# Optimization experiments

Measured on AMD Instinct MI355X. Metric: run time of the kernel, lower is better.

The kernel has to match this reference:

```python
import jax, jax.numpy as jnp
import numpy as np

N_NODES = 50000
N_EDGES = 800000
NUM_FEATURES = 256
HIDDEN = 256
HEADS = 8
OUT_DIM = 2


def setup_inputs() -> dict:
    key = jax.random.key(0)
    ks = jax.random.split(key, 16)
    C1 = HIDDEN // HEADS  # 32 per-head channels
    inp = {
        'x': jax.random.normal(ks[0], (N_NODES, NUM_FEATURES), dtype=jnp.float32),
        'edge_index': jax.random.randint(ks[1], (2, N_EDGES), 0, N_NODES, dtype=jnp.int64),
        # layer 1: num_features -> heads * (hidden//heads)
        'W1': jax.random.normal(ks[2], (NUM_FEATURES, HEADS * C1), dtype=jnp.float32) * 0.05,
        'att_src1': jax.random.normal(ks[3], (HEADS, C1), dtype=jnp.float32) * 0.1,
        'att_dst1': jax.random.normal(ks[4], (HEADS, C1), dtype=jnp.float32) * 0.1,
        'b1': jnp.zeros((HEADS * C1,), dtype=jnp.float32),
        # layer 2: hidden -> heads * (hidden//heads)
        'W2': jax.random.normal(ks[5], (HIDDEN, HEADS * C1), dtype=jnp.float32) * 0.05,
        'att_src2': jax.random.normal(ks[6], (HEADS, C1), dtype=jnp.float32) * 0.1,
        'att_dst2': jax.random.normal(ks[7], (HEADS, C1), dtype=jnp.float32) * 0.1,
        'b2': jnp.zeros((HEADS * C1,), dtype=jnp.float32),
        # layer 3: hidden -> output_dim, heads=1, concat=False
        'W3': jax.random.normal(ks[8], (HIDDEN, OUT_DIM), dtype=jnp.float32) * 0.05,
        'att_src3': jax.random.normal(ks[9], (1, OUT_DIM), dtype=jnp.float32) * 0.1,
        'att_dst3': jax.random.normal(ks[10], (1, OUT_DIM), dtype=jnp.float32) * 0.1,
        'b3': jnp.zeros((OUT_DIM,), dtype=jnp.float32),
    }
    return inp


def _gat_layer(x, src, dst, W, a_src, a_dst, b, concat):
    # PyG GATConv: h = x W -> [N, H, C]; e_ij = leaky_relu(a_src.h_j + a_dst.h_i)
    # softmax over edges grouped by destination, then scatter-add h_j * alpha.
    N = x.shape[0]
    H, C = a_src.shape
    h = (x @ W).reshape(N, H, C)
    alpha_s = jnp.einsum('nhc,hc->nh', h, a_src)  # [N, H]
    alpha_d = jnp.einsum('nhc,hc->nh', h, a_dst)
    e = jax.nn.leaky_relu(alpha_s[src] + alpha_d[dst], negative_slope=0.2)  # [E, H]
    m = jax.ops.segment_max(e, dst, num_segments=N)  # per-dst max for stable softmax
    ee = jnp.exp(e - m[dst])
    denom = jax.ops.segment_sum(ee, dst, num_segments=N)
    alpha = ee / (denom[dst] + 1e-16)  # [E, H]
    msg = h[src] * alpha[:, :, None]  # [E, H, C]
    out = jax.ops.segment_sum(msg, dst, num_segments=N)  # [N, H, C]
    out = out.reshape(N, H * C) if concat else out.mean(axis=1)
    return out + b


def reference(x, edge_index, W1, att_src1, att_dst1, b1, W2, att_src2, att_dst2, b2, W3, att_src3, att_dst3, b3):
    N = x.shape[0]
    loops = jnp.arange(N, dtype=edge_index.dtype)
    src = jnp.concatenate([edge_index[0], loops])  # PyG add_self_loops=True
    dst = jnp.concatenate([edge_index[1], loops])
    h = _gat_layer(x, src, dst, W1, att_src1, att_dst1, b1, concat=True)
    h = jax.nn.elu(h)  # dropout is identity in eval mode
    h = _gat_layer(h, src, dst, W2, att_src2, att_dst2, b2, concat=True)
    h = jax.nn.elu(h)
    out = _gat_layer(h, src, dst, W3, att_src3, att_dst3, b3, concat=False)
    return out  # [N, output_dim]; batch=None so pooling/MLP head is skipped
```

## Files before the change

### kernel.cpp

```cpp
#include <hip/hip_runtime.h>
#include <math.h>

#define NF 256
#define NHEADS 8
#define MNEG -1e30f

typedef _Float16 half8 __attribute__((ext_vector_type(8)));
typedef float f32x4 __attribute__((ext_vector_type(4)));


__global__ __launch_bounds__(256) void deg_count_k(const int* __restrict__ dst, int* __restrict__ deg, int E) {
    int i = (blockIdx.x * 256 + threadIdx.x) * 4;
    if (i + 4 <= E) {
        int4 d = *(const int4*)&dst[i];
        atomicAdd(&deg[d.x], 1);
        atomicAdd(&deg[d.y], 1);
        atomicAdd(&deg[d.z], 1);
        atomicAdd(&deg[d.w], 1);
    } else {
        for (int e = i; e < E; ++e) atomicAdd(&deg[dst[e]], 1);
    }
}

__global__ __launch_bounds__(256) void scan1_k(const int* __restrict__ deg, int* __restrict__ indptr,
                                               int* __restrict__ bsum, int n) {
    __shared__ int sh[256];
    int tid = threadIdx.x;
    int i = blockIdx.x * 256 + tid;
    int d = (i < n) ? deg[i] : 0;
    sh[tid] = d;
    __syncthreads();
#pragma unroll
    for (int off = 1; off < 256; off <<= 1) {
        int t = (tid >= off) ? sh[tid - off] : 0;
        __syncthreads();
        sh[tid] += t;
        __syncthreads();
    }
    if (i < n) indptr[i] = sh[tid] - d;
    if (tid == 255) bsum[blockIdx.x] = sh[255];
}

__global__ __launch_bounds__(256) void scan3_k(const int* __restrict__ deg, int* __restrict__ indptr,
                                               const int* __restrict__ bsum, int* __restrict__ cursor,
                                               int* __restrict__ srcs, int n, int nb) {
    __shared__ int sh[256];
    int tid = threadIdx.x;
    int d = (tid < nb) ? bsum[tid] : 0;
    sh[tid] = d;
    __syncthreads();
#pragma unroll
    for (int off = 1; off < 256; off <<= 1) {
        int t = (tid >= off) ? sh[tid - off] : 0;
        __syncthreads();
        sh[tid] += t;
        __syncthreads();
    }
    int bid = blockIdx.x;
    int boff = sh[bid] - ((bid < nb) ? bsum[bid] : 0);
    int i = bid * 256 + tid;
    if (i < n) {
        int v = indptr[i] + boff + i;
        indptr[i] = v;
        srcs[v] = i;
        cursor[i] = v + 1;
        if (i == n - 1) indptr[n] = v + deg[i] + 1;
    }
}

__global__ __launch_bounds__(256) void fill_edge_k(const int* __restrict__ esrc, const int* __restrict__ edst,
                                                   int* __restrict__ cursor, int* __restrict__ srcs, int E) {
    int i = (blockIdx.x * 256 + threadIdx.x) * 4;
    if (i + 4 <= E) {
        int4 s = *(const int4*)&esrc[i];
        int4 d = *(const int4*)&edst[i];
        srcs[atomicAdd(&cursor[d.x], 1)] = s.x;
        srcs[atomicAdd(&cursor[d.y], 1)] = s.y;
        srcs[atomicAdd(&cursor[d.z], 1)] = s.z;
        srcs[atomicAdd(&cursor[d.w], 1)] = s.w;
    } else {
        for (int e = i; e < E; ++e) srcs[atomicAdd(&cursor[edst[e]], 1)] = esrc[e];
    }
}


__global__ __launch_bounds__(256) void prep_w_k(const float* __restrict__ W1, const float* __restrict__ W2,
                                                _Float16* __restrict__ O1, _Float16* __restrict__ O2) {
    int tid = blockIdx.x * 256 + threadIdx.x;
    const float* W = (tid < 65536) ? W1 : W2;
    _Float16* O = (tid < 65536) ? O1 : O2;
    int t = tid & 65535;
    int k = t >> 8, c = t & 255;
    O[(size_t)c * 256 + k] = (_Float16)W[t];
}


template <int AF32>
__global__ __launch_bounds__(512, 4) void gemm_mfma_k(const void* __restrict__ Av, const _Float16* __restrict__ WTh,
                                                      const float* __restrict__ att_s, const float* __restrict__ att_d,
                                                      _Float16* __restrict__ C, float* __restrict__ aS,
                                                      float* __restrict__ aD, int M) {
    __shared__ __align__(16) _Float16 Asub[2][128][40];
    __shared__ __align__(16) _Float16 Wsub[2][256][40];
    int t = threadIdx.x;
    int wave = t >> 6, lane = t & 63;
    int wm = wave >> 2, wn = wave & 3;
    int lr = lane & 15, lg = lane >> 4;
    int r0 = blockIdx.x * 128;
    const float* Af = (const float*)Av;
    const _Float16* Ah = (const _Float16*)Av;

    int arow = t >> 2, aoff = (t & 3) * 8;
    int wcol = t >> 1, woff = (t & 1) * 16;
    int ga_row = r0 + arow; ga_row = ga_row < M ? ga_row : M - 1;

    half8 aR, wR0, wR1;
    {
        if (AF32) {
            const float* p = Af + (size_t)ga_row * 256 + aoff;
            float4 x0 = *(const float4*)p;
            float4 x1 = *(const float4*)(p + 4);
            aR[0] = (_Float16)x0.x; aR[1] = (_Float16)x0.y; aR[2] = (_Float16)x0.z; aR[3] = (_Float16)x0.w;
            aR[4] = (_Float16)x1.x; aR[5] = (_Float16)x1.y; aR[6] = (_Float16)x1.z; aR[7] = (_Float16)x1.w;
        } else {
            aR = *(const half8*)(Ah + (size_t)ga_row * 256 + aoff);
        }
        const _Float16* p = WTh + (size_t)wcol * 256 + woff;
        wR0 = *(const half8*)p;
        wR1 = *(const half8*)(p + 8);
    }
    *(half8*)&Asub[0][arow][aoff] = aR;
    *(half8*)&Wsub[0][wcol][woff] = wR0;
    *(half8*)&Wsub[0][wcol][woff + 8] = wR1;
    __syncthreads();

    f32x4 acc[4][4];
#pragma unroll
    for (int mr = 0; mr < 4; ++mr)
#pragma unroll
        for (int nr = 0; nr < 4; ++nr) acc[mr][nr] = (f32x4){0.f, 0.f, 0.f, 0.f};

#pragma unroll
    for (int ks = 0; ks < 8; ++ks) {
        int cur = ks & 1;
        if (ks < 7) {
            int k0 = (ks + 1) * 32;
            if (AF32) {
                const float* p = Af + (size_t)ga_row * 256 + k0 + aoff;
                float4 x0 = *(const float4*)p;
                float4 x1 = *(const float4*)(p + 4);
                aR[0] = (_Float16)x0.x; aR[1] = (_Float16)x0.y; aR[2] = (_Float16)x0.z; aR[3] = (_Float16)x0.w;
                aR[4] = (_Float16)x1.x; aR[5] = (_Float16)x1.y; aR[6] = (_Float16)x1.z; aR[7] = (_Float16)x1.w;
            } else {
                aR = *(const half8*)(Ah + (size_t)ga_row * 256 + k0 + aoff);
            }
            const _Float16* p = WTh + (size_t)wcol * 256 + k0 + woff;
            wR0 = *(const half8*)p;
            wR1 = *(const half8*)(p + 8);
        }
        {
            half8 a[4], b[4];
#pragma unroll
            for (int mr = 0; mr < 4; ++mr)
                a[mr] = *(const half8*)&Asub[cur][wm * 64 + mr * 16 + lr][lg * 8];
#pragma unroll
            for (int nr = 0; nr < 4; ++nr)
                b[nr] = *(const half8*)&Wsub[cur][wn * 64 + nr * 16 + lr][lg * 8];
#pragma unroll
            for (int mr = 0; mr < 4; ++mr)
#pragma unroll
                for (int nr = 0; nr < 4; ++nr)
                    acc[mr][nr] = __builtin_amdgcn_mfma_f32_16x16x32_f16(a[mr], b[nr], acc[mr][nr], 0, 0, 0);
        }
        if (ks < 7) {
            __syncthreads();
            *(half8*)&Asub[cur ^ 1][arow][aoff] = aR;
            *(half8*)&Wsub[cur ^ 1][wcol][woff] = wR0;
            *(half8*)&Wsub[cur ^ 1][wcol][woff + 8] = wR1;
            __syncthreads();
        }
    }

    int c0 = wn * 64;
    int h0 = wn * 2, h1 = wn * 2 + 1;
    float as_c0 = att_s[h0 * 32 + lr],      as_c1 = att_s[h0 * 32 + 16 + lr];
    float as_c2 = att_s[h1 * 32 + lr],      as_c3 = att_s[h1 * 32 + 16 + lr];
    float ad_c0 = att_d[h0 * 32 + lr],      ad_c1 = att_d[h0 * 32 + 16 + lr];
    float ad_c2 = att_d[h1 * 32 + lr],      ad_c3 = att_d[h1 * 32 + 16 + lr];

#pragma unroll
    for (int mr = 0; mr < 4; ++mr) {
        int rbase = r0 + wm * 64 + mr * 16 + lg * 4;
#pragma unroll
        for (int j = 0; j < 4; ++j) {
            int row = rbase + j;
            float ps0 = acc[mr][0][j] * as_c0 + acc[mr][1][j] * as_c1;
            float ps1 = acc[mr][2][j] * as_c2 + acc[mr][3][j] * as_c3;
            float pd0 = acc[mr][0][j] * ad_c0 + acc[mr][1][j] * ad_c1;
            float pd1 = acc[mr][2][j] * ad_c2 + acc[mr][3][j] * ad_c3;
#pragma unroll
            for (int o = 1; o < 16; o <<= 1) {
                ps0 += __shfl_xor(ps0, o);
                ps1 += __shfl_xor(ps1, o);
                pd0 += __shfl_xor(pd0, o);
                pd1 += __shfl_xor(pd1, o);
            }
            if (row < M) {
#pragma unroll
                for (int nr = 0; nr < 4; ++nr)
                    C[(size_t)row * 256 + c0 + nr * 16 + lr] = (_Float16)acc[mr][nr][j];
                if (lr == 0) {
                    aS[(size_t)row * NHEADS + h0] = ps0;
                    aS[(size_t)row * NHEADS + h1] = ps1;
                    aD[(size_t)row * NHEADS + h0] = pd0;
                    aD[(size_t)row * NHEADS + h1] = pd1;
                }
            }
        }
    }
}


template <int MODE>
__global__ __launch_bounds__(256) void agg_k(const _Float16* __restrict__ h, const float* __restrict__ aS,
                                             const float* __restrict__ aD, const int* __restrict__ indptr,
                                             const int* __restrict__ srcs, const float* __restrict__ bias,
                                             _Float16* __restrict__ out,
                                             const float* __restrict__ W3, const float* __restrict__ as3,
                                             const float* __restrict__ ad3, float* __restrict__ h3,
                                             float* __restrict__ s3, float* __restrict__ d3, int N) {
    int wid = blockIdx.x * 4 + (threadIdx.x >> 6);
    if (wid >= N) return;
    int lane = threadIdx.x & 63;
    int hf = lane >> 5;
    int cl = lane & 31;
    int hh = cl >> 2;
    float ad = aD[(size_t)wid * NHEADS + hh];
    int beg = indptr[wid], end = indptr[wid + 1];
    const half8* h8p = (const half8*)h;
    float m = MNEG, den = 0.f;
    float f0 = 0, f1 = 0, f2 = 0, f3 = 0, f4 = 0, f5 = 0, f6 = 0, f7 = 0;
    int k = beg;
    int sp[4];
    if (k + 8 <= end) {
#pragma unroll
        for (int j = 0; j < 4; ++j) sp[j] = srcs[k + 2 * j + hf];
    }
    for (; k + 8 <= end; k += 8) {
        int s[4]; float as[4]; half8 v[4]; float e[4];
#pragma unroll
        for (int j = 0; j < 4; ++j) s[j] = sp[j];
        if (k + 16 <= end) {
#pragma unroll
            for (int j = 0; j < 4; ++j) sp[j] = srcs[k + 8 + 2 * j + hf];
        }
#pragma unroll
        for (int j = 0; j < 4; ++j) as[j] = aS[(size_t)s[j] * NHEADS + hh];
#pragma unroll
        for (int j = 0; j < 4; ++j) v[j] = h8p[(size_t)s[j] * 32 + cl];
#pragma unroll
        for (int j = 0; j < 4; ++j) { e[j] = as[j] + ad; e[j] = fmaxf(e[j], 0.2f * e[j]); }
        float em = fmaxf(fmaxf(e[0], e[1]), fmaxf(e[2], e[3]));
        if (__any(em > m + 4.f)) {
            float mn = fmaxf(m, em);
            float sc = __expf(m - mn);
            den *= sc; f0 *= sc; f1 *= sc; f2 *= sc; f3 *= sc; f4 *= sc; f5 *= sc; f6 *= sc; f7 *= sc;
            m = mn;
        }
        half8 hacc = (half8)(_Float16)0.f;
#pragma unroll
        for (int j = 0; j < 4; ++j) {
            float p = __expf(e[j] - m);
            den += p;
            _Float16 ph = (_Float16)p;
            half8 pb = {ph, ph, ph, ph, ph, ph, ph, ph};
            hacc += v[j] * pb;
        }
        f0 += (float)hacc[0]; f1 += (float)hacc[1]; f2 += (float)hacc[2]; f3 += (float)hacc[3];
        f4 += (float)hacc[4]; f5 += (float)hacc[5]; f6 += (float)hacc[6]; f7 += (float)hacc[7];
    }
    for (; k + 2 <= end; k += 2) {
        int s = srcs[k + hf];
        float as = aS[(size_t)s * NHEADS + hh];
        half8 v = h8p[(size_t)s * 32 + cl];
        float e = as + ad; e = fmaxf(e, 0.2f * e);
        if (__any(e > m + 4.f)) {
            float mn = fmaxf(m, e);
            float sc = __expf(m - mn);
            den *= sc; f0 *= sc; f1 *= sc; f2 *= sc; f3 *= sc; f4 *= sc; f5 *= sc; f6 *= sc; f7 *= sc;
            m = mn;
        }
        float p = __expf(e - m);
        den += p;
        f0 += p * (float)v[0]; f1 += p * (float)v[1]; f2 += p * (float)v[2]; f3 += p * (float)v[3];
        f4 += p * (float)v[4]; f5 += p * (float)v[5]; f6 += p * (float)v[6]; f7 += p * (float)v[7];
    }
    if (k < end) {
        int s = srcs[k];
        float e = aS[(size_t)s * NHEADS + hh] + ad;
        e = fmaxf(e, 0.2f * e);
        half8 v = h8p[(size_t)s * 32 + cl];
        float eg = (hf == 0) ? e : MNEG;
        if (__any(eg > m + 4.f)) {
            float mn = fmaxf(m, eg);
            float sc = __expf(m - mn);
            den *= sc; f0 *= sc; f1 *= sc; f2 *= sc; f3 *= sc; f4 *= sc; f5 *= sc; f6 *= sc; f7 *= sc;
            m = mn;
        }
        float p = (hf == 0) ? __expf(e - m) : 0.f;
        den += p;
        f0 += p * (float)v[0]; f1 += p * (float)v[1]; f2 += p * (float)v[2]; f3 += p * (float)v[3];
        f4 += p * (float)v[4]; f5 += p * (float)v[5]; f6 += p * (float)v[6]; f7 += p * (float)v[7];
    }
    {
        float m2 = __shfl_xor(m, 32);
        float den2 = __shfl_xor(den, 32);
        float mn = fmaxf(m, m2);
        float sc1 = __expf(m - mn), sc2 = __expf(m2 - mn);
        den = den * sc1 + den2 * sc2;
        f0 = f0 * sc1 + __shfl_xor(f0, 32) * sc2;
        f1 = f1 * sc1 + __shfl_xor(f1, 32) * sc2;
        f2 = f2 * sc1 + __shfl_xor(f2, 32) * sc2;
        f3 = f3 * sc1 + __shfl_xor(f3, 32) * sc2;
        f4 = f4 * sc1 + __shfl_xor(f4, 32) * sc2;
        f5 = f5 * sc1 + __shfl_xor(f5, 32) * sc2;
        f6 = f6 * sc1 + __shfl_xor(f6, 32) * sc2;
        f7 = f7 * sc1 + __shfl_xor(f7, 32) * sc2;
    }
    float inv = 1.f / (den + 1e-16f);
    float4 bv0 = *(const float4*)&bias[cl * 8];
    float4 bv1 = *(const float4*)&bias[cl * 8 + 4];
    float o[8];
    o[0] = f0 * inv + bv0.x; o[1] = f1 * inv + bv0.y; o[2] = f2 * inv + bv0.z; o[3] = f3 * inv + bv0.w;
    o[4] = f4 * inv + bv1.x; o[5] = f5 * inv + bv1.y; o[6] = f6 * inv + bv1.z; o[7] = f7 * inv + bv1.w;
#pragma unroll
    for (int c = 0; c < 8; ++c) o[c] = (o[c] > 0.f) ? o[c] : expm1f(o[c]);

    if (MODE == 0) {
        if (hf == 0) {
            half8 ov;
#pragma unroll
            for (int c = 0; c < 8; ++c) ov[c] = (_Float16)o[c];
            ((half8*)out)[(size_t)wid * 32 + cl] = ov;
        }
    } else {
        const float4* W34 = (const float4*)W3;
        float p0 = 0.f, p1 = 0.f;
#pragma unroll
        for (int q = 0; q < 4; ++q) {
            float4 w = W34[cl * 4 + q];
            p0 += o[2 * q] * w.x + o[2 * q + 1] * w.z;
            p1 += o[2 * q] * w.y + o[2 * q + 1] * w.w;
        }
#pragma unroll
        for (int off = 1; off < 32; off <<= 1) {
            p0 += __shfl_xor(p0, off);
            p1 += __shfl_xor(p1, off);
        }
        if (lane == 0) {
            h3[(size_t)wid * 2] = p0;
            h3[(size_t)wid * 2 + 1] = p1;
            s3[wid] = p0 * as3[0] + p1 * as3[1];
            d3[wid] = p0 * ad3[0] + p1 * ad3[1];
        }
    }
}


__global__ __launch_bounds__(256) void agg3_k(const float* __restrict__ h3, const float* __restrict__ s3,
                                              const float* __restrict__ d3, const int* __restrict__ indptr,
                                              const int* __restrict__ srcs, const float* __restrict__ b3,
                                              float* __restrict__ out, int N) {
    int t = blockIdx.x * 256 + threadIdx.x;
    int n = t >> 2;
    if (n >= N) return;
    int sub = t & 3;
    float ad = d3[n];
    float m = MNEG, den = 0.f, a0 = 0.f, a1 = 0.f;
    int beg = indptr[n], end = indptr[n + 1];
    for (int k = beg + sub; k < end; k += 4) {
        int s = srcs[k];
        float e = s3[s] + ad;
        e = fmaxf(e, 0.2f * e);
        if (e > m + 8.f) {
            float mn = fmaxf(m, e);
            float sc = __expf(m - mn);
            den *= sc; a0 *= sc; a1 *= sc;
            m = mn;
        }
        float p = __expf(e - m);
        den += p;
        a0 += p * h3[(size_t)s * 2];
        a1 += p * h3[(size_t)s * 2 + 1];
    }
#pragma unroll
    for (int off = 1; off < 4; off <<= 1) {
        float m2 = __shfl_xor(m, off);
        float den2 = __shfl_xor(den, off);
        float a02 = __shfl_xor(a0, off);
        float a12 = __shfl_xor(a1, off);
        float mn = fmaxf(m, m2);
        float sc1 = __expf(m - mn);
        float sc2 = __expf(m2 - mn);
        den = den * sc1 + den2 * sc2;
        a0 = a0 * sc1 + a02 * sc2;
        a1 = a1 * sc1 + a12 * sc2;
        m = mn;
    }
    if (sub == 0) {
        float inv = 1.f / (den + 1e-16f);
        out[(size_t)n * 2]     = a0 * inv + b3[0];
        out[(size_t)n * 2 + 1] = a1 * inv + b3[1];
    }
}


extern "C" void kernel_launch(void* const* d_in, const int* in_sizes, int n_in,
                              void* d_out, int out_size, void* d_ws, size_t ws_size,
                              hipStream_t stream) {
    const float* x   = (const float*)d_in[0];
    const int*   ei  = (const int*)d_in[1];
    const float* W1  = (const float*)d_in[2];
    const float* as1 = (const float*)d_in[3];
    const float* ad1 = (const float*)d_in[4];
    const float* b1  = (const float*)d_in[5];
    const float* W2  = (const float*)d_in[6];
    const float* as2 = (const float*)d_in[7];
    const float* ad2 = (const float*)d_in[8];
    const float* b2  = (const float*)d_in[9];
    const float* W3  = (const float*)d_in[10];
    const float* at_s3 = (const float*)d_in[11];
    const float* at_d3 = (const float*)d_in[12];
    const float* b3  = (const float*)d_in[13];

    int N = in_sizes[0] / NF;
    int E = in_sizes[1] / 2;
    const int* esrc = ei;
    const int* edst = ei + E;

    char* w = (char*)d_ws;
    _Float16* hbuf  = (_Float16*)w; w += (size_t)N * NF * 2;
    _Float16* xnext = (_Float16*)w; w += (size_t)N * NF * 2;
    float* aS    = (float*)w; w += (size_t)N * NHEADS * 4;
    float* aD    = (float*)w; w += (size_t)N * NHEADS * 4;
    float* h3    = (float*)w; w += (size_t)N * 2 * 4;
    float* s3    = (float*)w; w += (size_t)N * 4;
    float* d3    = (float*)w; w += (size_t)N * 4;
    int* deg     = (int*)w; w += (size_t)N * 4;
    int* indptr  = (int*)w; w += (size_t)(N + 1) * 4 + 60;
    int* cursor  = (int*)w; w += (size_t)N * 4;
    int* bsum    = (int*)w; w += 256 * 4;
    _Float16* WTh1 = (_Float16*)w; w += (size_t)256 * 256 * 2;
    _Float16* WTh2 = (_Float16*)w; w += (size_t)256 * 256 * 2;
    int* srcs    = (int*)w;

    int nb_n = (N + 255) / 256;
    int nb_e4 = (E + 1023) / 1024;
    int nb_w = (N + 3) / 4;
    int nb_gm = (N + 127) / 128;
    int nb_a3 = (N * 4 + 255) / 256;

    hipMemsetAsync(deg, 0, (size_t)N * 4, stream);
    deg_count_k<<<nb_e4, 256, 0, stream>>>(edst, deg, E);
    scan1_k<<<nb_n, 256, 0, stream>>>(deg, indptr, bsum, N);
    scan3_k<<<nb_n, 256, 0, stream>>>(deg, indptr, bsum, cursor, srcs, N, nb_n);
    fill_edge_k<<<nb_e4, 256, 0, stream>>>(esrc, edst, cursor, srcs, E);
    prep_w_k<<<512, 256, 0, stream>>>(W1, W2, WTh1, WTh2);

    gemm_mfma_k<1><<<nb_gm, 512, 0, stream>>>(x, WTh1, as1, ad1, hbuf, aS, aD, N);
    agg_k<0><<<nb_w, 256, 0, stream>>>(hbuf, aS, aD, indptr, srcs, b1, xnext,
                                       nullptr, nullptr, nullptr, nullptr, nullptr, nullptr, N);
    gemm_mfma_k<0><<<nb_gm, 512, 0, stream>>>(xnext, WTh2, as2, ad2, hbuf, aS, aD, N);
    agg_k<1><<<nb_w, 256, 0, stream>>>(hbuf, aS, aD, indptr, srcs, b2, nullptr,
                                       W3, at_s3, at_d3, h3, s3, d3, N);
    agg3_k<<<nb_a3, 256, 0, stream>>>(h3, s3, d3, indptr, srcs, b3, (float*)d_out, N);
}
```

Before: 293.5 us.

## Merge graph-build kernels into weight prep and GEMM, prefetch aS in aggregation

Degree counting and weight transpose/convert share one launch via block-index dispatch. The CSR edge fill now runs as extra blocks of the layer-1 GEMM grid, so it overlaps with the matmul and saves two launches. The aggregation loop also prefetches the source attention scores one iteration ahead to hide gather latency. The cost is more code paths in the GEMM kernel and some added register pressure in the aggregation loop.

```diff
diff --git a/kernel.cpp b/kernel.cpp
--- a/kernel.cpp
+++ b/kernel.cpp
@@ -9,16 +9,28 @@
 typedef float f32x4 __attribute__((ext_vector_type(4)));
 
 
-__global__ __launch_bounds__(256) void deg_count_k(const int* __restrict__ dst, int* __restrict__ deg, int E) {
-    int i = (blockIdx.x * 256 + threadIdx.x) * 4;
-    if (i + 4 <= E) {
-        int4 d = *(const int4*)&dst[i];
-        atomicAdd(&deg[d.x], 1);
-        atomicAdd(&deg[d.y], 1);
-        atomicAdd(&deg[d.z], 1);
-        atomicAdd(&deg[d.w], 1);
+__global__ __launch_bounds__(256) void misc_k(const int* __restrict__ edst, int* __restrict__ deg, int E, int nbE,
+                                              const float* __restrict__ W1, const float* __restrict__ W2,
+                                              _Float16* __restrict__ O1, _Float16* __restrict__ O2) {
+    int bid = blockIdx.x;
+    if (bid < nbE) {
+        int i = (bid * 256 + threadIdx.x) * 4;
+        if (i + 4 <= E) {
+            int4 d = *(const int4*)&edst[i];
+            atomicAdd(&deg[d.x], 1);
+            atomicAdd(&deg[d.y], 1);
+            atomicAdd(&deg[d.z], 1);
+            atomicAdd(&deg[d.w], 1);
+        } else {
+            for (int e = i; e < E; ++e) atomicAdd(&deg[edst[e]], 1);
+        }
     } else {
-        for (int e = i; e < E; ++e) atomicAdd(&deg[dst[e]], 1);
+        int tid = (bid - nbE) * 256 + threadIdx.x;
+        const float* W = (tid < 65536) ? W1 : W2;
+        _Float16* O = (tid < 65536) ? O1 : O2;
+        int t = tid & 65535;
+        int k = t >> 8, c = t & 255;
+        O[(size_t)c * 256 + k] = (_Float16)W[t];
     }
 }
 
@@ -68,40 +80,31 @@
     }
 }
 
-__global__ __launch_bounds__(256) void fill_edge_k(const int* __restrict__ esrc, const int* __restrict__ edst,
-                                                   int* __restrict__ cursor, int* __restrict__ srcs, int E) {
-    int i = (blockIdx.x * 256 + threadIdx.x) * 4;
-    if (i + 4 <= E) {
-        int4 s = *(const int4*)&esrc[i];
-        int4 d = *(const int4*)&edst[i];
-        srcs[atomicAdd(&cursor[d.x], 1)] = s.x;
-        srcs[atomicAdd(&cursor[d.y], 1)] = s.y;
-        srcs[atomicAdd(&cursor[d.z], 1)] = s.z;
-        srcs[atomicAdd(&cursor[d.w], 1)] = s.w;
-    } else {
-        for (int e = i; e < E; ++e) srcs[atomicAdd(&cursor[edst[e]], 1)] = esrc[e];
-    }
-}
-
-
-__global__ __launch_bounds__(256) void prep_w_k(const float* __restrict__ W1, const float* __restrict__ W2,
-                                                _Float16* __restrict__ O1, _Float16* __restrict__ O2) {
-    int tid = blockIdx.x * 256 + threadIdx.x;
-    const float* W = (tid < 65536) ? W1 : W2;
-    _Float16* O = (tid < 65536) ? O1 : O2;
-    int t = tid & 65535;
-    int k = t >> 8, c = t & 255;
-    O[(size_t)c * 256 + k] = (_Float16)W[t];
-}
-
 
 template <int AF32>
 __global__ __launch_bounds__(512, 4) void gemm_mfma_k(const void* __restrict__ Av, const _Float16* __restrict__ WTh,
                                                       const float* __restrict__ att_s, const float* __restrict__ att_d,
                                                       _Float16* __restrict__ C, float* __restrict__ aS,
-                                                      float* __restrict__ aD, int M) {
+                                                      float* __restrict__ aD, int M,
+                                                      const int* __restrict__ esrc, const int* __restrict__ edst,
+                                                      int* __restrict__ cursor, int* __restrict__ srcs,
+                                                      int E, int GB) {
     __shared__ __align__(16) _Float16 Asub[2][128][40];
     __shared__ __align__(16) _Float16 Wsub[2][256][40];
+    if (blockIdx.x >= GB) {
+        int i = ((blockIdx.x - GB) * 512 + threadIdx.x) * 4;
+        if (i + 4 <= E) {
+            int4 s = *(const int4*)&esrc[i];
+            int4 d = *(const int4*)&edst[i];
+            srcs[atomicAdd(&cursor[d.x], 1)] = s.x;
+            srcs[atomicAdd(&cursor[d.y], 1)] = s.y;
+            srcs[atomicAdd(&cursor[d.z], 1)] = s.z;
+            srcs[atomicAdd(&cursor[d.w], 1)] = s.w;
+        } else {
+            for (int e = i; e < E; ++e) srcs[atomicAdd(&cursor[edst[e]], 1)] = esrc[e];
+        }
+        return;
+    }
     int t = threadIdx.x;
     int wave = t >> 6, lane = t & 63;
     int wm = wave >> 2, wn = wave & 3;
@@ -241,23 +244,27 @@
     float m = MNEG, den = 0.f;
     float f0 = 0, f1 = 0, f2 = 0, f3 = 0, f4 = 0, f5 = 0, f6 = 0, f7 = 0;
     int k = beg;
-    int sp[4];
+    int sp[4]; float asp[4];
     if (k + 8 <= end) {
 #pragma unroll
         for (int j = 0; j < 4; ++j) sp[j] = srcs[k + 2 * j + hf];
+#pragma unroll
+        for (int j = 0; j < 4; ++j) asp[j] = aS[(size_t)sp[j] * NHEADS + hh];
     }
     for (; k + 8 <= end; k += 8) {
         int s[4]; float as[4]; half8 v[4]; float e[4];
 #pragma unroll
-        for (int j = 0; j < 4; ++j) s[j] = sp[j];
+        for (int j = 0; j < 4; ++j) { s[j] = sp[j]; as[j] = asp[j]; }
         if (k + 16 <= end) {
 #pragma unroll
             for (int j = 0; j < 4; ++j) sp[j] = srcs[k + 8 + 2 * j + hf];
         }
 #pragma unroll
-        for (int j = 0; j < 4; ++j) as[j] = aS[(size_t)s[j] * NHEADS + hh];
-#pragma unroll
         for (int j = 0; j < 4; ++j) v[j] = h8p[(size_t)s[j] * 32 + cl];
+        if (k + 16 <= end) {
+#pragma unroll
+            for (int j = 0; j < 4; ++j) asp[j] = aS[(size_t)sp[j] * NHEADS + hh];
+        }
 #pragma unroll
         for (int j = 0; j < 4; ++j) { e[j] = as[j] + ad; e[j] = fmaxf(e[j], 0.2f * e[j]); }
         float em = fmaxf(fmaxf(e[0], e[1]), fmaxf(e[2], e[3]));
@@ -456,21 +463,22 @@
 
     int nb_n = (N + 255) / 256;
     int nb_e4 = (E + 1023) / 1024;
+    int nb_f  = (E + 2047) / 2048;
     int nb_w = (N + 3) / 4;
     int nb_gm = (N + 127) / 128;
     int nb_a3 = (N * 4 + 255) / 256;
 
     hipMemsetAsync(deg, 0, (size_t)N * 4, stream);
-    deg_count_k<<<nb_e4, 256, 0, stream>>>(edst, deg, E);
+    misc_k<<<nb_e4 + 512, 256, 0, stream>>>(edst, deg, E, nb_e4, W1, W2, WTh1, WTh2);
     scan1_k<<<nb_n, 256, 0, stream>>>(deg, indptr, bsum, N);
     scan3_k<<<nb_n, 256, 0, stream>>>(deg, indptr, bsum, cursor, srcs, N, nb_n);
-    fill_edge_k<<<nb_e4, 256, 0, stream>>>(esrc, edst, cursor, srcs, E);
-    prep_w_k<<<512, 256, 0, stream>>>(W1, W2, WTh1, WTh2);
-
-    gemm_mfma_k<1><<<nb_gm, 512, 0, stream>>>(x, WTh1, as1, ad1, hbuf, aS, aD, N);
+
+    gemm_mfma_k<1><<<nb_gm + nb_f, 512, 0, stream>>>(x, WTh1, as1, ad1, hbuf, aS, aD, N,
+                                                     esrc, edst, cursor, srcs, E, nb_gm);
     agg_k<0><<<nb_w, 256, 0, stream>>>(hbuf, aS, aD, indptr, srcs, b1, xnext,
                                        nullptr, nullptr, nullptr, nullptr, nullptr, nullptr, N);
-    gemm_mfma_k<0><<<nb_gm, 512, 0, stream>>>(xnext, WTh2, as2, ad2, hbuf, aS, aD, N);
+    gemm_mfma_k<0><<<nb_gm, 512, 0, stream>>>(xnext, WTh2, as2, ad2, hbuf, aS, aD, N,
+                                              nullptr, nullptr, nullptr, nullptr, 0, nb_gm);
     agg_k<1><<<nb_w, 256, 0, stream>>>(hbuf, aS, aD, indptr, srcs, b2, nullptr,
                                        W3, at_s3, at_d3, h3, s3, d3, N);
     agg3_k<<<nb_a3, 256, 0, stream>>>(h3, s3, d3, indptr, srcs, b3, (float*)d_out, N);
```

Measured after the change: 273.1 us. 1.07x faster.
